# Optimization experiments

Measured on AMD Instinct MI355X. Metric: run time of the kernel, lower is better.

## Reference

```python
import jax, jax.numpy as jnp
import numpy as np

L, B, A, I, H = 128, 128, 512, 512, 1024


def setup_inputs() -> dict:
    key = jax.random.key(0)
    ks = jax.random.split(key, 8)
    s = 0.02
    return {
        "action_features": jax.random.normal(ks[0], (L, B, A), jnp.float32),
        "input_feature": jax.random.normal(ks[1], (B, I), jnp.float32),
        "hidden_state": jax.random.normal(ks[2], (B, H), jnp.float32) * s,
        "state": jax.random.normal(ks[3], (B, H), jnp.float32) * s,
        "W_ih": jax.random.normal(ks[4], (4 * H, I + A), jnp.float32) * s,
        "W_hh": jax.random.normal(ks[5], (4 * H, H), jnp.float32) * s,
        "b_ih": jax.random.normal(ks[6], (4 * H,), jnp.float32) * s,
        "b_hh": jax.random.normal(ks[7], (4 * H,), jnp.float32) * s,
    }


def reference(action_features, input_feature, hidden_state, state, W_ih, W_hh, b_ih, b_hh):
    # x_t = concat(input_feature, a_t); precompute the input-side gate projection
    # for all timesteps in one big GEMM: [L,B,I+A] @ [I+A,4H] -> [L,B,4H]
    x = jnp.concatenate(
        [jnp.broadcast_to(input_feature, (action_features.shape[0],) + input_feature.shape),
         action_features], axis=-1)
    gates_x = jnp.einsum('lbi,gi->lbg', x, W_ih) + b_ih + b_hh

    def step(carry, gx):
        h, c = carry
        gates = gx + h @ W_hh.T  # [B, 4H]
        i_g, f_g, g_g, o_g = jnp.split(gates, 4, axis=-1)
        c1 = jax.nn.sigmoid(f_g) * c + jax.nn.sigmoid(i_g) * jnp.tanh(g_g)
        h1 = jax.nn.sigmoid(o_g) * jnp.tanh(c1)
        return (h1, c1), h1

    (h_n, c_n), hs = jax.lax.scan(step, (hidden_state, state), gates_x)
    return hs, h_n, c_n
```

## Files before the change

kernel.cpp:

```cpp
#include <hip/hip_runtime.h>
#include <hip/hip_bf16.h>

#define LL 128
#define BB 128
#define AA 512
#define II 512
#define HH 1024
#define KK 1024
#define NTEAM 8
#define NDG 32
#define NBLK (NTEAM * NDG)

typedef __attribute__((ext_vector_type(8))) short short8;
typedef __attribute__((ext_vector_type(4))) float f32x4;
typedef __attribute__((ext_vector_type(4))) unsigned uint32x4;

static __device__ __forceinline__ unsigned short f2b(float x) {
    union { float f; unsigned u; } v; v.f = x;
    unsigned r = v.u + 0x7fffu + ((v.u >> 16) & 1u);
    return (unsigned short)(r >> 16);
}
static __device__ __forceinline__ float fast_sigmoid(float x) {
    return 1.f / (1.f + __expf(-x));
}
static __device__ __forceinline__ float fast_tanh(float x) {
    float e = __expf(2.f * x);
    return (e - 1.f) / (e + 1.f);
}

static __device__ __forceinline__ short8 uc_load128(const unsigned short* p) {
    short8 r;
    asm volatile("global_load_dwordx4 %0, %1, off sc0 sc1" : "=v"(r) : "v"(p));
    return r;
}
static __device__ __forceinline__ void uc_store128(unsigned short* p, uint32x4 v) {
    asm volatile("global_store_dwordx4 %0, %1, off sc0 sc1" :: "v"(p), "v"(v) : "memory");
}
static __device__ __forceinline__ unsigned uc_flag_load(const unsigned int* p) {
    unsigned fv;
    asm volatile("global_load_dword %0, %1, off sc0 sc1\n\ts_waitcnt vmcnt(0)"
                 : "=v"(fv) : "v"(p) : "memory");
    return fv;
}
static __device__ __forceinline__ void uc_flag_store(unsigned int* p, unsigned v) {
    asm volatile("global_store_dword %0, %1, off sc0 sc1" :: "v"(p), "v"(v) : "memory");
}

__global__ void cast_kernel(const float* __restrict__ s, unsigned short* __restrict__ d, int n) {
    int stride = gridDim.x * blockDim.x;
    for (int i = blockIdx.x * blockDim.x + threadIdx.x; i < n; i += stride) d[i] = f2b(s[i]);
}

__launch_bounds__(512, 2)
__global__ void lstm_kernel(const unsigned short* __restrict__ xa,
                            const float* __restrict__ inF,
                            const float* __restrict__ Wih,
                            const float* __restrict__ Whh,
                            const float* __restrict__ bih,
                            const float* __restrict__ bhh,
                            const float* __restrict__ c0,
                            unsigned short* __restrict__ hb,
                            unsigned int* __restrict__ flagsG,
                            float* __restrict__ out) {
    __shared__ __attribute__((aligned(16))) unsigned short wa_lds[8 * 16 * 64 * 8];
    __shared__ float red[2 * 3 * 64 * 17];
    __shared__ __attribute__((aligned(16))) unsigned short hbuf[16 * 32];

    const int tid  = threadIdx.x;
    const int lane = tid & 63;
    const int w    = tid >> 6;
    const int nq   = w >> 2;
    const int ksl  = w & 3;
    const int dg   = blockIdx.x & (NDG - 1);
    const int mg   = blockIdx.x >> 5;
    const int j0   = dg * 32;
    const int b0   = mg * 16;
    const int d    = lane & 15;
    const int rg   = lane >> 4;

    short8 breg[4][8];
    #pragma unroll
    for (int t = 0; t < 4; ++t) {
        #pragma unroll
        for (int kf = 0; kf < 8; ++kf) {
            const float* src = &Whh[(size_t)(t * HH + j0 + nq * 16 + d) * HH + ksl * 256 + kf * 32 + rg * 8];
            short8 v;
            #pragma unroll
            for (int j = 0; j < 8; ++j) v[j] = (short)f2b(src[j]);
            breg[t][kf] = v;
        }
    }

    #pragma unroll
    for (int t = 0; t < 4; ++t) {
        #pragma unroll
        for (int kf = 0; kf < 4; ++kf) {
            const float* src = &Wih[(size_t)(t * HH + j0 + nq * 16 + d) * KK + II + ksl * 128 + kf * 32 + rg * 8];
            unsigned short* dst = &wa_lds[(((size_t)w * 16 + t * 4 + kf) * 64 + lane) * 8];
            #pragma unroll
            for (int j = 0; j < 8; ++j) dst[j] = f2b(src[j]);
        }
    }

    f32x4 bacc[4] = {};
    #pragma unroll
    for (int kf = 0; kf < 4; ++kf) {
        const float* xs = &inF[(size_t)(b0 + d) * II + ksl * 128 + kf * 32 + rg * 8];
        short8 xf;
        #pragma unroll
        for (int j = 0; j < 8; ++j) xf[j] = (short)f2b(xs[j]);
        #pragma unroll
        for (int t = 0; t < 4; ++t) {
            const float* ws = &Wih[(size_t)(t * HH + j0 + nq * 16 + d) * KK + ksl * 128 + kf * 32 + rg * 8];
            short8 wf;
            #pragma unroll
            for (int j = 0; j < 8; ++j) wf[j] = (short)f2b(ws[j]);
            bacc[t] = __builtin_amdgcn_mfma_f32_16x16x32_bf16(xf, wf, bacc[t], 0, 0, 0);
        }
    }
    if (ksl != 0) {
        float* sp = &red[(size_t)((nq * 3 + (ksl - 1)) * 64 + lane) * 17];
        #pragma unroll
        for (int t = 0; t < 4; ++t)
            #pragma unroll
            for (int r = 0; r < 4; ++r) sp[t * 4 + r] = bacc[t][r];
    }
    __syncthreads();
    float base_r[16], c_r[4];
    if (ksl == 0) {
        #pragma unroll
        for (int s = 0; s < 3; ++s) {
            const float* sp = &red[(size_t)((nq * 3 + s) * 64 + lane) * 17];
            #pragma unroll
            for (int t = 0; t < 4; ++t)
                #pragma unroll
                for (int r = 0; r < 4; ++r) bacc[t][r] += sp[t * 4 + r];
        }
        #pragma unroll
        for (int t = 0; t < 4; ++t) {
            float bias = bih[t * HH + j0 + nq * 16 + d] + bhh[t * HH + j0 + nq * 16 + d];
            #pragma unroll
            for (int r = 0; r < 4; ++r) base_r[t * 4 + r] = bacc[t][r] + bias;
        }
        #pragma unroll
        for (int r = 0; r < 4; ++r) c_r[r] = c0[(b0 + rg * 4 + r) * HH + j0 + nq * 16 + d];
    }
    __syncthreads();

    unsigned int*       ourflag  = flagsG + mg * NDG + dg;
    const unsigned int* pollflag = flagsG + mg * NDG + (lane & 31);

    for (int l = 0; l < LL; ++l) {
        const unsigned short* hr = hb + (size_t)(l & 1) * (BB * HH);
        unsigned short*       hw = hb + (size_t)((l + 1) & 1) * (BB * HH);

        f32x4 acc[4] = {};
        {
            const unsigned short* ap = xa + ((size_t)l * BB + b0 + d) * AA + ksl * 128 + rg * 8;
            short8 aaf[4];
            #pragma unroll
            for (int kf = 0; kf < 4; ++kf) aaf[kf] = *(const short8*)(ap + kf * 32);
            #pragma unroll
            for (int kf = 0; kf < 4; ++kf)
                #pragma unroll
                for (int t = 0; t < 4; ++t) {
                    short8 wfr = *(const short8*)&wa_lds[(((size_t)w * 16 + t * 4 + kf) * 64 + lane) * 8];
                    acc[t] = __builtin_amdgcn_mfma_f32_16x16x32_bf16(aaf[kf], wfr, acc[t], 0, 0, 0);
                }
        }

        if (l > 0 && w == 7) {
            unsigned fv; int guard = 0;
            do { fv = uc_flag_load(pollflag); }
            while (__any(fv < (unsigned)l) && ++guard < (1 << 18));
        }
        __syncthreads();

        short8 af[8];
        const unsigned short* hp = hr + (size_t)(b0 + d) * HH + ksl * 256 + rg * 8;
        #pragma unroll
        for (int kf = 0; kf < 8; ++kf) af[kf] = uc_load128(hp + kf * 32);
        asm volatile("s_waitcnt vmcnt(0)" ::: "memory");
        __builtin_amdgcn_sched_barrier(0);

        #pragma unroll
        for (int kf = 0; kf < 8; ++kf)
            #pragma unroll
            for (int t = 0; t < 4; ++t)
                acc[t] = __builtin_amdgcn_mfma_f32_16x16x32_bf16(af[kf], breg[t][kf], acc[t], 0, 0, 0);

        if (ksl != 0) {
            float* sp = &red[(size_t)((nq * 3 + (ksl - 1)) * 64 + lane) * 17];
            #pragma unroll
            for (int t = 0; t < 4; ++t)
                #pragma unroll
                for (int r = 0; r < 4; ++r) sp[t * 4 + r] = acc[t][r];
        }
        __syncthreads();

        float h1v[4];
        if (ksl == 0) {
            #pragma unroll
            for (int s = 0; s < 3; ++s) {
                const float* sp = &red[(size_t)((nq * 3 + s) * 64 + lane) * 17];
                #pragma unroll
                for (int t = 0; t < 4; ++t)
                    #pragma unroll
                    for (int r = 0; r < 4; ++r) acc[t][r] += sp[t * 4 + r];
            }
            #pragma unroll
            for (int r = 0; r < 4; ++r) {
                float gi = acc[0][r] + base_r[0 + r];
                float gf = acc[1][r] + base_r[4 + r];
                float gg = acc[2][r] + base_r[8 + r];
                float go = acc[3][r] + base_r[12 + r];
                float ig = fast_sigmoid(gi);
                float fg = fast_sigmoid(gf);
                float og = fast_sigmoid(go);
                float gt = fast_tanh(gg);
                float c1 = fg * c_r[r] + ig * gt;
                float h1 = og * fast_tanh(c1);
                c_r[r] = c1;
                h1v[r] = h1;
                hbuf[(rg * 4 + r) * 32 + nq * 16 + d] = f2b(h1);
            }
        }
        __syncthreads();

        if (w == 2 && l < LL - 1) {
            int row = lane >> 2, ch = lane & 3;
            uint32x4 hv = *(const uint32x4*)&hbuf[row * 32 + ch * 8];
            uc_store128(&hw[(size_t)(b0 + row) * HH + j0 + ch * 8], hv);
            asm volatile("s_waitcnt vmcnt(0)" ::: "memory");
            if (lane == 0) uc_flag_store(ourflag, (unsigned)(l + 1));
        }

        if (ksl == 0) {
            #pragma unroll
            for (int r = 0; r < 4; ++r)
                out[((size_t)l * BB + (b0 + rg * 4 + r)) * HH + j0 + nq * 16 + d] = h1v[r];
            if (l == LL - 1) {
                #pragma unroll
                for (int r = 0; r < 4; ++r) {
                    out[(size_t)LL * BB * HH + (b0 + rg * 4 + r) * HH + j0 + nq * 16 + d] = h1v[r];
                    out[(size_t)LL * BB * HH + BB * HH + (b0 + rg * 4 + r) * HH + j0 + nq * 16 + d] = c_r[r];
                }
            }
        }
    }
}

extern "C" void kernel_launch(void* const* d_in, const int* in_sizes, int n_in,
                              void* d_out, int out_size, void* d_ws, size_t ws_size,
                              hipStream_t stream) {
    const float* act = (const float*)d_in[0];
    const float* inF = (const float*)d_in[1];
    const float* h0  = (const float*)d_in[2];
    const float* c0  = (const float*)d_in[3];
    const float* Wih = (const float*)d_in[4];
    const float* Whh = (const float*)d_in[5];
    const float* bih = (const float*)d_in[6];
    const float* bhh = (const float*)d_in[7];
    float* out = (float*)d_out;

    char* p = (char*)d_ws;
    unsigned short* xa    = (unsigned short*)p; p += (size_t)LL * BB * AA * 2;
    unsigned short* hb    = (unsigned short*)p; p += (size_t)2 * BB * HH * 2;
    unsigned int*   flags = (unsigned int*)p;   p += NTEAM * NDG * sizeof(unsigned int);

    hipMemsetAsync(flags, 0, NTEAM * NDG * sizeof(unsigned int), stream);
    cast_kernel<<<dim3(2048), dim3(256), 0, stream>>>(act, xa, LL * BB * AA);
    cast_kernel<<<dim3(64), dim3(256), 0, stream>>>(h0, hb, BB * HH);

    void* args[] = { (void*)&xa, (void*)&inF, (void*)&Wih, (void*)&Whh, (void*)&bih,
                     (void*)&bhh, (void*)&c0, (void*)&hb, (void*)&flags, (void*)&out };
    hipLaunchCooperativeKernel((const void*)lstm_kernel, dim3(NBLK), dim3(512), args, 0, stream);
}
```

Before: 781.9 us.

## Embed step parity in bf16 hidden-state LSB to drop store-wait before flag

```diff
diff --git a/kernel.cpp b/kernel.cpp
--- a/kernel.cpp
+++ b/kernel.cpp
@@ -10,6 +10,7 @@
 #define NTEAM 8
 #define NDG 32
 #define NBLK (NTEAM * NDG)
+#define HROT 3
 
 typedef __attribute__((ext_vector_type(8))) short short8;
 typedef __attribute__((ext_vector_type(4))) float f32x4;
@@ -19,6 +20,9 @@
     union { float f; unsigned u; } v; v.f = x;
     unsigned r = v.u + 0x7fffu + ((v.u >> 16) & 1u);
     return (unsigned short)(r >> 16);
+}
+static __device__ __forceinline__ unsigned short f2b_par(float x, unsigned p) {
+    return (unsigned short)((f2b(x) & 0xFFFEu) | p);
 }
 static __device__ __forceinline__ float fast_sigmoid(float x) {
     return 1.f / (1.f + __expf(-x));
@@ -49,6 +53,18 @@
 __global__ void cast_kernel(const float* __restrict__ s, unsigned short* __restrict__ d, int n) {
     int stride = gridDim.x * blockDim.x;
     for (int i = blockIdx.x * blockDim.x + threadIdx.x; i < n; i += stride) d[i] = f2b(s[i]);
+}
+__global__ void cast_par0_kernel(const float* __restrict__ s, unsigned short* __restrict__ d, int n) {
+    int stride = gridDim.x * blockDim.x;
+    for (int i = blockIdx.x * blockDim.x + threadIdx.x; i < n; i += stride)
+        d[i] = (unsigned short)(f2b(s[i]) & 0xFFFEu);
+}
+__global__ void fill_kernel(unsigned short* __restrict__ b1, unsigned short* __restrict__ b2, int n) {
+    int stride = gridDim.x * blockDim.x;
+    for (int i = blockIdx.x * blockDim.x + threadIdx.x; i < n; i += stride) {
+        b1[i] = 0x0000u;
+        b2[i] = 0x0001u;
+    }
 }
 
 __launch_bounds__(512, 2)
@@ -59,7 +75,7 @@
                             const float* __restrict__ bih,
                             const float* __restrict__ bhh,
                             const float* __restrict__ c0,
-                            unsigned short* __restrict__ hb,
+                            unsigned short* __restrict__ hbr,
                             unsigned int* __restrict__ flagsG,
                             float* __restrict__ out) {
     __shared__ __attribute__((aligned(16))) unsigned short wa_lds[8 * 16 * 64 * 8];
@@ -151,8 +167,8 @@
     const unsigned int* pollflag = flagsG + mg * NDG + (lane & 31);
 
     for (int l = 0; l < LL; ++l) {
-        const unsigned short* hr = hb + (size_t)(l & 1) * (BB * HH);
-        unsigned short*       hw = hb + (size_t)((l + 1) & 1) * (BB * HH);
+        const unsigned short* hr = hbr + (size_t)(l % HROT) * (BB * HH);
+        unsigned short*       hw = hbr + (size_t)((l + 1) % HROT) * (BB * HH);
 
         f32x4 acc[4] = {};
         {
@@ -177,10 +193,24 @@
         __syncthreads();
 
         short8 af[8];
-        const unsigned short* hp = hr + (size_t)(b0 + d) * HH + ksl * 256 + rg * 8;
-        #pragma unroll
-        for (int kf = 0; kf < 8; ++kf) af[kf] = uc_load128(hp + kf * 32);
-        asm volatile("s_waitcnt vmcnt(0)" ::: "memory");
+        {
+            const unsigned short* hp = hr + (size_t)(b0 + d) * HH + ksl * 256 + rg * 8;
+            const unsigned pp = (l & 1) ? 0x00010001u : 0u;
+            int guard = 0;
+            while (true) {
+                #pragma unroll
+                for (int kf = 0; kf < 8; ++kf) af[kf] = uc_load128(hp + kf * 32);
+                asm volatile("s_waitcnt vmcnt(0)" ::: "memory");
+                __builtin_amdgcn_sched_barrier(0);
+                unsigned bad = 0;
+                #pragma unroll
+                for (int kf = 0; kf < 8; ++kf) {
+                    uint32x4 u = __builtin_bit_cast(uint32x4, af[kf]);
+                    bad |= ((u[0] ^ pp) | (u[1] ^ pp) | (u[2] ^ pp) | (u[3] ^ pp)) & 0x00010001u;
+                }
+                if (!__any(bad != 0) || ++guard >= (1 << 16)) break;
+            }
+        }
         __builtin_amdgcn_sched_barrier(0);
 
         #pragma unroll
@@ -208,6 +238,7 @@
                     #pragma unroll
                     for (int r = 0; r < 4; ++r) acc[t][r] += sp[t * 4 + r];
             }
+            const unsigned p1 = (unsigned)((l + 1) & 1);
             #pragma unroll
             for (int r = 0; r < 4; ++r) {
                 float gi = acc[0][r] + base_r[0 + r];
@@ -222,7 +253,7 @@
                 float h1 = og * fast_tanh(c1);
                 c_r[r] = c1;
                 h1v[r] = h1;
-                hbuf[(rg * 4 + r) * 32 + nq * 16 + d] = f2b(h1);
+                hbuf[(rg * 4 + r) * 32 + nq * 16 + d] = f2b_par(h1, p1);
             }
         }
         __syncthreads();
@@ -231,7 +262,6 @@
             int row = lane >> 2, ch = lane & 3;
             uint32x4 hv = *(const uint32x4*)&hbuf[row * 32 + ch * 8];
             uc_store128(&hw[(size_t)(b0 + row) * HH + j0 + ch * 8], hv);
-            asm volatile("s_waitcnt vmcnt(0)" ::: "memory");
             if (lane == 0) uc_flag_store(ourflag, (unsigned)(l + 1));
         }
 
@@ -265,14 +295,16 @@
 
     char* p = (char*)d_ws;
     unsigned short* xa    = (unsigned short*)p; p += (size_t)LL * BB * AA * 2;
-    unsigned short* hb    = (unsigned short*)p; p += (size_t)2 * BB * HH * 2;
+    unsigned short* hbr   = (unsigned short*)p; p += (size_t)HROT * BB * HH * 2;
     unsigned int*   flags = (unsigned int*)p;   p += NTEAM * NDG * sizeof(unsigned int);
 
     hipMemsetAsync(flags, 0, NTEAM * NDG * sizeof(unsigned int), stream);
     cast_kernel<<<dim3(2048), dim3(256), 0, stream>>>(act, xa, LL * BB * AA);
-    cast_kernel<<<dim3(64), dim3(256), 0, stream>>>(h0, hb, BB * HH);
+    cast_par0_kernel<<<dim3(64), dim3(256), 0, stream>>>(h0, hbr, BB * HH);
+    fill_kernel<<<dim3(64), dim3(256), 0, stream>>>(hbr + (size_t)BB * HH,
+                                                    hbr + (size_t)2 * BB * HH, BB * HH);
 
     void* args[] = { (void*)&xa, (void*)&inF, (void*)&Wih, (void*)&Whh, (void*)&bih,
-                     (void*)&bhh, (void*)&c0, (void*)&hb, (void*)&flags, (void*)&out };
+                     (void*)&bhh, (void*)&c0, (void*)&hbr, (void*)&flags, (void*)&out };
     hipLaunchCooperativeKernel((const void*)lstm_kernel, dim3(NBLK), dim3(512), args, 0, stream);
 }
```

Result: slower. 801.4 us (+2.5%).

## Pre-cast LSTM weights to bf16 in separate kernels and pipeline flag polling

Applied to the files above, without the earlier changes.

```diff
diff --git a/kernel.cpp b/kernel.cpp
--- a/kernel.cpp
+++ b/kernel.cpp
@@ -36,12 +36,6 @@
 static __device__ __forceinline__ void uc_store128(unsigned short* p, uint32x4 v) {
     asm volatile("global_store_dwordx4 %0, %1, off sc0 sc1" :: "v"(p), "v"(v) : "memory");
 }
-static __device__ __forceinline__ unsigned uc_flag_load(const unsigned int* p) {
-    unsigned fv;
-    asm volatile("global_load_dword %0, %1, off sc0 sc1\n\ts_waitcnt vmcnt(0)"
-                 : "=v"(fv) : "v"(p) : "memory");
-    return fv;
-}
 static __device__ __forceinline__ void uc_flag_store(unsigned int* p, unsigned v) {
     asm volatile("global_store_dword %0, %1, off sc0 sc1" :: "v"(p), "v"(v) : "memory");
 }
@@ -54,8 +48,8 @@
 __launch_bounds__(512, 2)
 __global__ void lstm_kernel(const unsigned short* __restrict__ xa,
                             const float* __restrict__ inF,
-                            const float* __restrict__ Wih,
-                            const float* __restrict__ Whh,
+                            const unsigned short* __restrict__ wihb,
+                            const unsigned short* __restrict__ whhb,
                             const float* __restrict__ bih,
                             const float* __restrict__ bhh,
                             const float* __restrict__ c0,
@@ -82,23 +76,16 @@
     #pragma unroll
     for (int t = 0; t < 4; ++t) {
         #pragma unroll
-        for (int kf = 0; kf < 8; ++kf) {
-            const float* src = &Whh[(size_t)(t * HH + j0 + nq * 16 + d) * HH + ksl * 256 + kf * 32 + rg * 8];
-            short8 v;
-            #pragma unroll
-            for (int j = 0; j < 8; ++j) v[j] = (short)f2b(src[j]);
-            breg[t][kf] = v;
-        }
+        for (int kf = 0; kf < 8; ++kf)
+            breg[t][kf] = *(const short8*)&whhb[(size_t)(t * HH + j0 + nq * 16 + d) * HH + ksl * 256 + kf * 32 + rg * 8];
     }
 
     #pragma unroll
     for (int t = 0; t < 4; ++t) {
         #pragma unroll
         for (int kf = 0; kf < 4; ++kf) {
-            const float* src = &Wih[(size_t)(t * HH + j0 + nq * 16 + d) * KK + II + ksl * 128 + kf * 32 + rg * 8];
-            unsigned short* dst = &wa_lds[(((size_t)w * 16 + t * 4 + kf) * 64 + lane) * 8];
-            #pragma unroll
-            for (int j = 0; j < 8; ++j) dst[j] = f2b(src[j]);
+            short8 v = *(const short8*)&wihb[(size_t)(t * HH + j0 + nq * 16 + d) * KK + II + ksl * 128 + kf * 32 + rg * 8];
+            *(short8*)&wa_lds[(((size_t)w * 16 + t * 4 + kf) * 64 + lane) * 8] = v;
         }
     }
 
@@ -111,10 +98,7 @@
         for (int j = 0; j < 8; ++j) xf[j] = (short)f2b(xs[j]);
         #pragma unroll
         for (int t = 0; t < 4; ++t) {
-            const float* ws = &Wih[(size_t)(t * HH + j0 + nq * 16 + d) * KK + ksl * 128 + kf * 32 + rg * 8];
-            short8 wf;
-            #pragma unroll
-            for (int j = 0; j < 8; ++j) wf[j] = (short)f2b(ws[j]);
+            short8 wf = *(const short8*)&wihb[(size_t)(t * HH + j0 + nq * 16 + d) * KK + ksl * 128 + kf * 32 + rg * 8];
             bacc[t] = __builtin_amdgcn_mfma_f32_16x16x32_bf16(xf, wf, bacc[t], 0, 0, 0);
         }
     }
@@ -170,9 +154,21 @@
         }
 
         if (l > 0 && w == 7) {
-            unsigned fv; int guard = 0;
-            do { fv = uc_flag_load(pollflag); }
-            while (__any(fv < (unsigned)l) && ++guard < (1 << 18));
+            const unsigned lim = (unsigned)l;
+            unsigned fa, fb; int guard = 0;
+            asm volatile("global_load_dword %0, %1, off sc0 sc1" : "=v"(fa) : "v"(pollflag) : "memory");
+            __builtin_amdgcn_s_sleep(8);
+            for (;;) {
+                asm volatile("global_load_dword %0, %1, off sc0 sc1" : "=v"(fb) : "v"(pollflag) : "memory");
+                asm volatile("s_waitcnt vmcnt(1)" ::: "memory");
+                __builtin_amdgcn_sched_barrier(0);
+                if (!__any(fa < lim) || ++guard >= (1 << 18)) break;
+                asm volatile("global_load_dword %0, %1, off sc0 sc1" : "=v"(fa) : "v"(pollflag) : "memory");
+                asm volatile("s_waitcnt vmcnt(1)" ::: "memory");
+                __builtin_amdgcn_sched_barrier(0);
+                if (!__any(fb < lim) || ++guard >= (1 << 18)) break;
+            }
+            asm volatile("s_waitcnt vmcnt(0)" ::: "memory");
         }
         __syncthreads();
 
@@ -265,14 +261,18 @@
 
     char* p = (char*)d_ws;
     unsigned short* xa    = (unsigned short*)p; p += (size_t)LL * BB * AA * 2;
+    unsigned short* wihb  = (unsigned short*)p; p += (size_t)4 * HH * KK * 2;
+    unsigned short* whhb  = (unsigned short*)p; p += (size_t)4 * HH * HH * 2;
     unsigned short* hb    = (unsigned short*)p; p += (size_t)2 * BB * HH * 2;
     unsigned int*   flags = (unsigned int*)p;   p += NTEAM * NDG * sizeof(unsigned int);
 
     hipMemsetAsync(flags, 0, NTEAM * NDG * sizeof(unsigned int), stream);
     cast_kernel<<<dim3(2048), dim3(256), 0, stream>>>(act, xa, LL * BB * AA);
+    cast_kernel<<<dim3(1024), dim3(256), 0, stream>>>(Wih, wihb, 4 * HH * KK);
+    cast_kernel<<<dim3(1024), dim3(256), 0, stream>>>(Whh, whhb, 4 * HH * HH);
     cast_kernel<<<dim3(64), dim3(256), 0, stream>>>(h0, hb, BB * HH);
 
-    void* args[] = { (void*)&xa, (void*)&inF, (void*)&Wih, (void*)&Whh, (void*)&bih,
+    void* args[] = { (void*)&xa, (void*)&inF, (void*)&wihb, (void*)&whhb, (void*)&bih,
                      (void*)&bhh, (void*)&c0, (void*)&hb, (void*)&flags, (void*)&out };
     hipLaunchCooperativeKernel((const void*)lstm_kernel, dim3(NBLK), dim3(512), args, 0, stream);
 }
```

Measured after the change: 765.2 us (median of 3 runs). -2.1%, faster.
